# Optimization experiments

Measured on AMD Instinct MI355X. Metric: run time of the kernel, lower is better.

## Reference

```python
import jax, jax.numpy as jnp
import numpy as np

B, T, L, H, W = 8, 30000, 6, 128, 128
D_IN, C_DIM, HID, Z_DIM = 3, 32, 256, 128
MAX_DIM = 0.55


def setup_inputs() -> dict:
    key = jax.random.key(0)
    ks = jax.random.split(key, 12)
    p = jax.random.uniform(ks[0], (B, T, D_IN), dtype=jnp.float32)
    z = jax.random.normal(ks[1], (B, Z_DIM), dtype=jnp.float32)
    c = jax.random.normal(ks[2], (B, L, H, W, C_DIM), dtype=jnp.float32)
    # camera-like matrices: small rotation rows so projected coords stay in [-1, 1]
    C_mat = (jax.random.uniform(ks[3], (B, L, 4, 3), dtype=jnp.float32) - 0.5) * 0.3
    C_mat = C_mat.at[:, :, 3, :].set(1.0)  # row used as projection denominator
    fc_p_w = jax.random.normal(ks[4], (HID, D_IN), dtype=jnp.float32) * 0.1
    fc_p_b = jnp.zeros((HID,), jnp.float32)
    blk0_w0 = jax.random.normal(ks[5], (C_DIM, HID), dtype=jnp.float32) * 0.05
    blk0_b0 = jnp.zeros((C_DIM,), jnp.float32)
    blk0_w1 = jax.random.normal(ks[6], (C_DIM, C_DIM), dtype=jnp.float32) * 0.1
    blk0_b1 = jnp.zeros((C_DIM,), jnp.float32)
    blk0_ws = jax.random.normal(ks[7], (C_DIM, HID), dtype=jnp.float32) * 0.05
    blk_w0 = jax.random.normal(ks[8], (4, C_DIM, C_DIM), dtype=jnp.float32) * 0.1
    blk_b0 = jnp.zeros((4, C_DIM), jnp.float32)
    blk_w1 = jax.random.normal(ks[9], (4, C_DIM, C_DIM), dtype=jnp.float32) * 0.1
    blk_b1 = jnp.zeros((4, C_DIM), jnp.float32)
    fc_out_w = jax.random.normal(ks[10], (1, C_DIM), dtype=jnp.float32) * 0.1
    fc_out_b = jnp.zeros((1,), jnp.float32)
    return dict(p=p, z=z, c=c, C_mat=C_mat, fc_p_w=fc_p_w, fc_p_b=fc_p_b,
                blk0_w0=blk0_w0, blk0_b0=blk0_b0, blk0_w1=blk0_w1, blk0_b1=blk0_b1,
                blk0_ws=blk0_ws, blk_w0=blk_w0, blk_b0=blk_b0, blk_w1=blk_w1,
                blk_b1=blk_b1, fc_out_w=fc_out_w, fc_out_b=fc_out_b)


def _bilinear(p, c, C_mat):
    # p: [B,T,3], c: [B,L,H,W,D], C_mat: [B,L,4,3]
    Bb, Ll, Hh, Ww, Dd = c.shape
    interval = 2.0 / (Hh - 1)
    pp = p / MAX_DIM
    # proj[b,l,t,i] = sum_j C_mat[b,l,i,j] * pp[b,t,j]
    proj = jnp.einsum('blij,btj->blti', C_mat[:, :, :3, :], pp)
    denom = C_mat[:, :, 3, 0] + 0.05                      # [B,L]
    proj = proj / denom[:, :, None, None]
    xy = (proj[..., :2] + 1.0) / interval                 # [B,L,T,2]
    x, y = xy[..., 0], xy[..., 1]
    x0f, x1f = jnp.floor(x), jnp.ceil(x)
    y0f, y1f = jnp.floor(y), jnp.ceil(y)
    dx = (x1f - x)[..., None]                             # [B,L,T,1]
    dy = (y1f - y)[..., None]
    x0 = jnp.clip(x0f.astype(jnp.int32), 0, Hh - 1)
    x1 = jnp.clip(x1f.astype(jnp.int32), 0, Hh - 1)
    y0 = jnp.clip(y0f.astype(jnp.int32), 0, Ww - 1)
    y1 = jnp.clip(y1f.astype(jnp.int32), 0, Ww - 1)
    bi = jnp.arange(Bb)[:, None, None]
    li = jnp.arange(Ll)[None, :, None]
    f11 = c[bi, li, x0, y0]                               # [B,L,T,D]
    f12 = c[bi, li, x1, y0]
    f21 = c[bi, li, x0, y1]
    f22 = c[bi, li, x1, y1]
    interp = (f11 * dx * dy + f12 * (1 - dx) * dy
              + f21 * dx * (1 - dy) + f22 * (1 - dx) * (1 - dy))
    return interp.sum(axis=1)                             # sum over views -> [B,T,D]


def reference(p, z, c, C_mat, fc_p_w, fc_p_b, blk0_w0, blk0_b0, blk0_w1, blk0_b1,
              blk0_ws, blk_w0, blk_b0, blk_w1, blk_b1, fc_out_w, fc_out_b):
    feat = _bilinear(p, c, C_mat)                         # [B,T,32]
    net = p @ fc_p_w.T + fc_p_b                           # 1x1 conv == linear, [B,T,256]
    # block0 (256 -> 32, with linear shortcut)
    h = jax.nn.relu(net) @ blk0_w0.T + blk0_b0
    dx_ = jax.nn.relu(h) @ blk0_w1.T + blk0_b1
    net = net @ blk0_ws.T + dx_
    net = net + feat
    # blocks 1..4 (32 -> 32, identity shortcut)
    for i in range(4):
        h = jax.nn.relu(net) @ blk_w0[i].T + blk_b0[i]
        net = net + (jax.nn.relu(h) @ blk_w1[i].T + blk_b1[i])
        net = net + feat
    out = jax.nn.relu(net) @ fc_out_w.T + fc_out_b        # [B,T,1]
    return out[..., 0]                                    # [B,T]
```

## Files before the change

### kernel.cpp

```cpp
#include <hip/hip_runtime.h>

#define NB 8
#define NT 30000
#define NL 6
#define NC 32
#define NHID 256

typedef _Float16 f16;
typedef f16 half8 __attribute__((ext_vector_type(8)));
typedef f16 half4v __attribute__((ext_vector_type(4)));
typedef f16 half2v __attribute__((ext_vector_type(2)));
typedef float floatx4 __attribute__((ext_vector_type(4)));

__device__ __forceinline__ int permrow(int m) {
    return 8 * ((m & 15) >> 2) + 4 * (m >> 4) + (m & 3);
}

__device__ __forceinline__ half2v cvt2(float a, float b) {
    return __builtin_bit_cast(half2v, __builtin_amdgcn_cvt_pkrtz(a, b));
}

__device__ __forceinline__ half8 relupack2(floatx4 a, floatx4 b) {
    half2v p0 = cvt2(fmaxf(a[0], 0.f), fmaxf(a[1], 0.f));
    half2v p1 = cvt2(fmaxf(a[2], 0.f), fmaxf(a[3], 0.f));
    half2v p2 = cvt2(fmaxf(b[0], 0.f), fmaxf(b[1], 0.f));
    half2v p3 = cvt2(fmaxf(b[2], 0.f), fmaxf(b[3], 0.f));
    half4v q0 = __builtin_shufflevector(p0, p1, 0, 1, 2, 3);
    half4v q1 = __builtin_shufflevector(p2, p3, 0, 1, 2, 3);
    return __builtin_shufflevector(q0, q1, 0, 1, 2, 3, 4, 5, 6, 7);
}

__device__ __forceinline__ half8 zext4(half4v lo) {
    const half4v zh = {};
    return __builtin_shufflevector(lo, zh, 0, 1, 2, 3, 4, 5, 6, 7);
}

__global__ void fold_kernel(const float* __restrict__ ws, const float* __restrict__ fpw,
                            const float* __restrict__ fpb, floatx4* __restrict__ out) {
    __shared__ floatx4 s_part[8][32];
    int tid = threadIdx.x;
    int i = tid & 31, kc = tid >> 5;
    const float* wrow = ws + i * 256 + kc * 32;
    const float* pw = fpw + kc * 96;
    const float* pb = fpb + kc * 32;
    floatx4 acc = {};
    #pragma unroll 8
    for (int k = 0; k < 32; k++) {
        float w = wrow[k];
        acc[0] = fmaf(w, pw[k * 3 + 0], acc[0]);
        acc[1] = fmaf(w, pw[k * 3 + 1], acc[1]);
        acc[2] = fmaf(w, pw[k * 3 + 2], acc[2]);
        acc[3] = fmaf(w, pb[k], acc[3]);
    }
    s_part[kc][i] = acc;
    __syncthreads();
    if (kc == 0) {
        floatx4 s = s_part[0][i];
        #pragma unroll
        for (int j = 1; j < 8; j++) s += s_part[j][i];
        out[i] = s;
    }
}

__launch_bounds__(256, 2)
__global__ void decoder_kernel(
    const float* __restrict__ p, const float* __restrict__ c, const float* __restrict__ Cm,
    const float* __restrict__ fpw, const float* __restrict__ fpb,
    const float* __restrict__ b0w0, const float* __restrict__ b0b0,
    const float* __restrict__ b0w1, const float* __restrict__ b0b1,
    const float* __restrict__ bw0, const float* __restrict__ bb0,
    const float* __restrict__ bw1, const float* __restrict__ bb1,
    const float* __restrict__ fow, const float* __restrict__ fob,
    const floatx4* __restrict__ fold, float* __restrict__ out)
{
    __shared__ __align__(16) f16 s_w0A[32 * 256];
    __shared__ __align__(16) f16 s_wA[9 * 32 * 32];
    __shared__ __align__(16) f16 s_hB[256 * 4];
    __shared__ __align__(16) f16 s_foldA[32 * 4];
    __shared__ __align__(16) float s_b0b0[32], s_fow[32];
    __shared__ __align__(16) float s_bb0f[128], s_bb1f[128];
    __shared__ float s_cam[NL][8];
    __shared__ float s_fob;

    const int tid = threadIdx.x;
    const int b = blockIdx.y;

    {
        int m = tid >> 3, seg = tid & 7;
        const float* src = b0w0 + permrow(m) * 256 + seg * 32;
        f16* dst = s_w0A + m * 256;
        int sw = m & 7;
        #pragma unroll
        for (int ci = 0; ci < 4; ci++) {
            int cidx = seg * 4 + ci;
            floatx4 f0 = *(const floatx4*)(src + ci * 8);
            floatx4 f1 = *(const floatx4*)(src + ci * 8 + 4);
            half2v h0 = cvt2(f0[0], f0[1]), h1 = cvt2(f0[2], f0[3]);
            half2v h2 = cvt2(f1[0], f1[1]), h3 = cvt2(f1[2], f1[3]);
            half4v q0 = __builtin_shufflevector(h0, h1, 0, 1, 2, 3);
            half4v q1 = __builtin_shufflevector(h2, h3, 0, 1, 2, 3);
            half8 h = __builtin_shufflevector(q0, q1, 0, 1, 2, 3, 4, 5, 6, 7);
            *(half8*)(dst + ((cidx ^ sw) << 3)) = h;
        }
    }
    for (int r = tid; r < 288; r += 256) {
        int mi = r >> 5, m = r & 31;
        int pm = permrow(m);
        const float* src;
        if (mi == 0) src = b0w1 + pm * 32;
        else {
            int mat = mi - 1, bi = mat >> 1;
            src = ((mat & 1) ? bw1 : bw0) + (bi * 32 + pm) * 32;
        }
        f16* dst = s_wA + mi * 1024 + m * 32;
        int sw = (m >> 1) & 3;
        #pragma unroll
        for (int ci = 0; ci < 4; ci++) {
            floatx4 f0 = *(const floatx4*)(src + ci * 8);
            floatx4 f1 = *(const floatx4*)(src + ci * 8 + 4);
            half2v h0 = cvt2(f0[0], f0[1]), h1 = cvt2(f0[2], f0[3]);
            half2v h2 = cvt2(f1[0], f1[1]), h3 = cvt2(f1[2], f1[3]);
            half4v q0 = __builtin_shufflevector(h0, h1, 0, 1, 2, 3);
            half4v q1 = __builtin_shufflevector(h2, h3, 0, 1, 2, 3);
            half8 h = __builtin_shufflevector(q0, q1, 0, 1, 2, 3, 4, 5, 6, 7);
            *(half8*)(dst + ((ci ^ sw) << 3)) = h;
        }
    }
    {
        int cch = tid >> 5, m = tid & 31;
        int h = cch * 32 + permrow(m);
        half2v a = cvt2(fpw[h * 3 + 0], fpw[h * 3 + 1]);
        half2v bq = cvt2(fpw[h * 3 + 2], fpb[h]);
        *(half4v*)(s_hB + tid * 4) = __builtin_shufflevector(a, bq, 0, 1, 2, 3);
    }
    if (tid < 32) {
        int pm = permrow(tid);
        floatx4 f = fold[pm];
        half2v a = cvt2(f[0], f[1]);
        half2v bq = cvt2(f[2], f[3] + b0b1[pm]);
        *(half4v*)(s_foldA + tid * 4) = __builtin_shufflevector(a, bq, 0, 1, 2, 3);
        s_b0b0[tid] = b0b0[tid];
        s_fow[tid]  = fow[tid];
    }
    if (tid >= 64 && tid < 192) {
        int j = tid - 64;
        s_bb0f[j] = bb0[j];
        s_bb1f[j] = bb1[j];
    }
    if (tid == 0) s_fob = fob[0];
    if (tid >= 192 && tid < 192 + NL) {
        int l = tid - 192;
        const float* cm = Cm + ((size_t)b * NL + l) * 12;
        float denom = cm[9] + 0.05f;
        float s = 63.5f / (0.55f * denom);
        s_cam[l][0] = cm[0] * s; s_cam[l][1] = cm[1] * s; s_cam[l][2] = cm[2] * s;
        s_cam[l][3] = cm[3] * s; s_cam[l][4] = cm[4] * s; s_cam[l][5] = cm[5] * s;
    }
    __syncthreads();

    const int lane = tid & 63;
    const int wv = tid >> 6;
    const int q = lane >> 4;
    const int i16 = lane & 15;
    const int sw0 = i16 & 7;

    const f16* w0r0 = s_w0A + i16 * 256;
    const f16* w0r1 = s_w0A + (16 + i16) * 256;
    const int qsw = (q ^ ((i16 >> 1) & 3)) << 3;
    const int soff0 = i16 * 32 + qsw;
    const int soff1 = (16 + i16) * 32 + qsw;
    const f16* hB0 = s_hB + i16 * 4;
    const f16* hB1 = s_hB + (16 + i16) * 4;
    const float* cq = c + (((size_t)b * NL) << 19) + q * 8;

    const half8 fA0 = zext4(*(const half4v*)(s_foldA + i16 * 4));
    const half8 fA1 = zext4(*(const half4v*)(s_foldA + (16 + i16) * 4));
    const floatx4 fw0 = *(const floatx4*)&s_fow[q * 8];
    const floatx4 fw1 = *(const floatx4*)&s_fow[q * 8 + 4];
    const floatx4 b00a = *(const floatx4*)&s_b0b0[q * 8];
    const floatx4 b00b = *(const floatx4*)&s_b0b0[q * 8 + 4];

    #pragma unroll 1
    for (int g = 0; g < 2; g++) {
        const int t = blockIdx.x * 128 + (g * 4 + wv) * 16 + i16;
        const int tc = min(t, NT - 1);
        const float* pp = p + ((size_t)b * NT + tc) * 3;
        float px = pp[0], py = pp[1], pz = pp[2];

        floatx4 fe0 = {}, fe1 = {};
        #pragma unroll 1
        for (int l = 0; l < NL; l++) {
            float x = s_cam[l][0] * px + s_cam[l][1] * py + s_cam[l][2] * pz + 63.5f;
            float y = s_cam[l][3] * px + s_cam[l][4] * py + s_cam[l][5] * pz + 63.5f;
            float x0f = floorf(x), x1f = ceilf(x);
            float y0f = floorf(y), y1f = ceilf(y);
            float dxw = x1f - x, dyw = y1f - y;
            int x0 = min(max((int)x0f, 0), 127);
            int x1 = min(max((int)x1f, 0), 127);
            int y0 = min(max((int)y0f, 0), 127);
            int y1 = min(max((int)y1f, 0), 127);
            const float* base = cq + ((size_t)l << 19);
            const floatx4* f11 = (const floatx4*)(base + (size_t)((x0 << 7) + y0) * 32);
            const floatx4* f12 = (const floatx4*)(base + (size_t)((x1 << 7) + y0) * 32);
            const floatx4* f21 = (const floatx4*)(base + (size_t)((x0 << 7) + y1) * 32);
            const floatx4* f22 = (const floatx4*)(base + (size_t)((x1 << 7) + y1) * 32);
            float w11 = dxw * dyw;
            float w12 = (1.f - dxw) * dyw;
            float w21 = dxw * (1.f - dyw);
            float w22 = (1.f - dxw) * (1.f - dyw);
            floatx4 a0 = f11[0], a1 = f11[1];
            floatx4 b0v = f12[0], b1v = f12[1];
            floatx4 c0v = f21[0], c1v = f21[1];
            floatx4 d0v = f22[0], d1v = f22[1];
            fe0 += a0 * w11 + b0v * w12 + c0v * w21 + d0v * w22;
            fe1 += a1 * w11 + b1v * w12 + c1v * w21 + d1v * w22;
        }

        half8 bp;
        {
            half2v xy = cvt2(px, py), z1 = cvt2(pz, 1.0f);
            half4v lo = __builtin_shufflevector(xy, z1, 0, 1, 2, 3);
            half8 full = zext4(lo);
            const half8 zh8 = {};
            bp = (q == 0) ? full : zh8;
        }

        floatx4 acc0 = b00a, acc1 = b00b;
        #pragma unroll 2
        for (int cch = 0; cch < 8; cch++) {
            half8 ha = zext4(*(const half4v*)(hB0 + cch * 128));
            half8 hb = zext4(*(const half4v*)(hB1 + cch * 128));
            floatx4 hz = {};
            floatx4 h0 = __builtin_amdgcn_mfma_f32_16x16x32_f16(ha, bp, hz, 0, 0, 0);
            floatx4 h1 = __builtin_amdgcn_mfma_f32_16x16x32_f16(hb, bp, hz, 0, 0, 0);
            half8 bf = relupack2(h0, h1);
            half8 a0 = *(const half8*)(w0r0 + ((((cch << 2) | q) ^ sw0) << 3));
            half8 a1 = *(const half8*)(w0r1 + ((((cch << 2) | q) ^ sw0) << 3));
            acc0 = __builtin_amdgcn_mfma_f32_16x16x32_f16(a0, bf, acc0, 0, 0, 0);
            acc1 = __builtin_amdgcn_mfma_f32_16x16x32_f16(a1, bf, acc1, 0, 0, 0);
        }

        floatx4 st0 = __builtin_amdgcn_mfma_f32_16x16x32_f16(fA0, bp, fe0, 0, 0, 0);
        floatx4 st1 = __builtin_amdgcn_mfma_f32_16x16x32_f16(fA1, bp, fe1, 0, 0, 0);
        {
            half8 bf = relupack2(acc0, acc1);
            half8 a0 = *(const half8*)(s_wA + soff0);
            half8 a1 = *(const half8*)(s_wA + soff1);
            st0 = __builtin_amdgcn_mfma_f32_16x16x32_f16(a0, bf, st0, 0, 0, 0);
            st1 = __builtin_amdgcn_mfma_f32_16x16x32_f16(a1, bf, st1, 0, 0, 0);
        }

        #pragma unroll
        for (int bk = 0; bk < 4; bk++) {
            const f16* w_a = s_wA + (1 + 2 * bk) * 1024;
            const f16* w_b = s_wA + (2 + 2 * bk) * 1024;
            floatx4 h0 = *(const floatx4*)&s_bb0f[bk * 32 + q * 8];
            floatx4 h1 = *(const floatx4*)&s_bb0f[bk * 32 + q * 8 + 4];
            {
                half8 bf = relupack2(st0, st1);
                half8 a0 = *(const half8*)(w_a + soff0);
                half8 a1 = *(const half8*)(w_a + soff1);
                h0 = __builtin_amdgcn_mfma_f32_16x16x32_f16(a0, bf, h0, 0, 0, 0);
                h1 = __builtin_amdgcn_mfma_f32_16x16x32_f16(a1, bf, h1, 0, 0, 0);
            }
            floatx4 d0 = *(const floatx4*)&s_bb1f[bk * 32 + q * 8];
            floatx4 d1 = *(const floatx4*)&s_bb1f[bk * 32 + q * 8 + 4];
            {
                half8 bf = relupack2(h0, h1);
                half8 a0 = *(const half8*)(w_b + soff0);
                half8 a1 = *(const half8*)(w_b + soff1);
                d0 = __builtin_amdgcn_mfma_f32_16x16x32_f16(a0, bf, d0, 0, 0, 0);
                d1 = __builtin_amdgcn_mfma_f32_16x16x32_f16(a1, bf, d1, 0, 0, 0);
            }
            st0 += d0 + fe0;
            st1 += d1 + fe1;
        }

        float o = 0.f;
        #pragma unroll
        for (int r = 0; r < 4; r++)
            o += fmaxf(st0[r], 0.f) * fw0[r] + fmaxf(st1[r], 0.f) * fw1[r];
        o += __shfl_xor(o, 16);
        o += __shfl_xor(o, 32);
        if (q == 0 && t < NT) out[(size_t)b * NT + t] = o + s_fob;
    }
}

extern "C" void kernel_launch(void* const* d_in, const int* in_sizes, int n_in,
                              void* d_out, int out_size, void* d_ws, size_t ws_size,
                              hipStream_t stream) {
    const float* p    = (const float*)d_in[0];
    const float* c    = (const float*)d_in[2];
    const float* Cm   = (const float*)d_in[3];
    const float* fpw  = (const float*)d_in[4];
    const float* fpb  = (const float*)d_in[5];
    const float* b0w0 = (const float*)d_in[6];
    const float* b0b0 = (const float*)d_in[7];
    const float* b0w1 = (const float*)d_in[8];
    const float* b0b1 = (const float*)d_in[9];
    const float* b0ws = (const float*)d_in[10];
    const float* bw0  = (const float*)d_in[11];
    const float* bb0  = (const float*)d_in[12];
    const float* bw1  = (const float*)d_in[13];
    const float* bb1  = (const float*)d_in[14];
    const float* fow  = (const float*)d_in[15];
    const float* fob  = (const float*)d_in[16];
    floatx4* fold = (floatx4*)d_ws;

    fold_kernel<<<1, 256, 0, stream>>>(b0ws, fpw, fpb, fold);

    dim3 grid((NT + 127) / 128, NB);
    decoder_kernel<<<grid, 256, 0, stream>>>(p, c, Cm, fpw, fpb,
                                             b0w0, b0b0, b0w1, b0b1,
                                             bw0, bb0, bw1, bb1,
                                             fow, fob, fold, (float*)d_out);
}
```

Measured before the change: 267.4 us.

## Interleave two point groups per wave and fold shortcut weights in-kernel

Replaces the sequential two-iteration point loop with a single pass that processes both 16-point groups together, interleaving their bilinear gathers and MFMA chains to expose more memory and matrix-core parallelism. Also removes the separate fold_kernel launch by computing the folded shortcut/first-layer weights in every block's prologue, with an extra barrier. This raises register pressure and duplicates a small fold computation across all blocks.

```diff
diff --git a/kernel.cpp b/kernel.cpp
--- a/kernel.cpp
+++ b/kernel.cpp
@@ -35,31 +35,29 @@
     return __builtin_shufflevector(lo, zh, 0, 1, 2, 3, 4, 5, 6, 7);
 }
 
-__global__ void fold_kernel(const float* __restrict__ ws, const float* __restrict__ fpw,
-                            const float* __restrict__ fpb, floatx4* __restrict__ out) {
-    __shared__ floatx4 s_part[8][32];
-    int tid = threadIdx.x;
-    int i = tid & 31, kc = tid >> 5;
-    const float* wrow = ws + i * 256 + kc * 32;
-    const float* pw = fpw + kc * 96;
-    const float* pb = fpb + kc * 32;
-    floatx4 acc = {};
-    #pragma unroll 8
-    for (int k = 0; k < 32; k++) {
-        float w = wrow[k];
-        acc[0] = fmaf(w, pw[k * 3 + 0], acc[0]);
-        acc[1] = fmaf(w, pw[k * 3 + 1], acc[1]);
-        acc[2] = fmaf(w, pw[k * 3 + 2], acc[2]);
-        acc[3] = fmaf(w, pb[k], acc[3]);
-    }
-    s_part[kc][i] = acc;
-    __syncthreads();
-    if (kc == 0) {
-        floatx4 s = s_part[0][i];
-        #pragma unroll
-        for (int j = 1; j < 8; j++) s += s_part[j][i];
-        out[i] = s;
-    }
+__device__ __forceinline__ void gatherv(const float* __restrict__ base, float x, float y,
+                                        floatx4& f0, floatx4& f1) {
+    float x0f = floorf(x), x1f = ceilf(x);
+    float y0f = floorf(y), y1f = ceilf(y);
+    float dxw = x1f - x, dyw = y1f - y;
+    int x0 = min(max((int)x0f, 0), 127);
+    int x1 = min(max((int)x1f, 0), 127);
+    int y0 = min(max((int)y0f, 0), 127);
+    int y1 = min(max((int)y1f, 0), 127);
+    const floatx4* f11 = (const floatx4*)(base + (size_t)((x0 << 7) + y0) * 32);
+    const floatx4* f12 = (const floatx4*)(base + (size_t)((x1 << 7) + y0) * 32);
+    const floatx4* f21 = (const floatx4*)(base + (size_t)((x0 << 7) + y1) * 32);
+    const floatx4* f22 = (const floatx4*)(base + (size_t)((x1 << 7) + y1) * 32);
+    float w11 = dxw * dyw;
+    float w12 = (1.f - dxw) * dyw;
+    float w21 = dxw * (1.f - dyw);
+    float w22 = (1.f - dxw) * (1.f - dyw);
+    floatx4 a0 = f11[0], a1 = f11[1];
+    floatx4 b0v = f12[0], b1v = f12[1];
+    floatx4 c0v = f21[0], c1v = f21[1];
+    floatx4 d0v = f22[0], d1v = f22[1];
+    f0 += a0 * w11 + b0v * w12 + c0v * w21 + d0v * w22;
+    f1 += a1 * w11 + b1v * w12 + c1v * w21 + d1v * w22;
 }
 
 __launch_bounds__(256, 2)
@@ -68,15 +66,16 @@
     const float* __restrict__ fpw, const float* __restrict__ fpb,
     const float* __restrict__ b0w0, const float* __restrict__ b0b0,
     const float* __restrict__ b0w1, const float* __restrict__ b0b1,
-    const float* __restrict__ bw0, const float* __restrict__ bb0,
-    const float* __restrict__ bw1, const float* __restrict__ bb1,
-    const float* __restrict__ fow, const float* __restrict__ fob,
-    const floatx4* __restrict__ fold, float* __restrict__ out)
+    const float* __restrict__ b0ws, const float* __restrict__ bw0,
+    const float* __restrict__ bb0, const float* __restrict__ bw1,
+    const float* __restrict__ bb1, const float* __restrict__ fow,
+    const float* __restrict__ fob, float* __restrict__ out)
 {
     __shared__ __align__(16) f16 s_w0A[32 * 256];
     __shared__ __align__(16) f16 s_wA[9 * 32 * 32];
     __shared__ __align__(16) f16 s_hB[256 * 4];
     __shared__ __align__(16) f16 s_foldA[32 * 4];
+    __shared__ floatx4 s_part[8][32];
     __shared__ __align__(16) float s_b0b0[32], s_fow[32];
     __shared__ __align__(16) float s_bb0f[128], s_bb1f[128];
     __shared__ float s_cam[NL][8];
@@ -133,12 +132,23 @@
         half2v bq = cvt2(fpw[h * 3 + 2], fpb[h]);
         *(half4v*)(s_hB + tid * 4) = __builtin_shufflevector(a, bq, 0, 1, 2, 3);
     }
+    {
+        int i = tid & 31, kc = tid >> 5;
+        const float* wrow = b0ws + i * 256 + kc * 32;
+        const float* pw = fpw + kc * 96;
+        const float* pb = fpb + kc * 32;
+        floatx4 acc = {};
+        #pragma unroll 8
+        for (int k = 0; k < 32; k++) {
+            float w = wrow[k];
+            acc[0] = fmaf(w, pw[k * 3 + 0], acc[0]);
+            acc[1] = fmaf(w, pw[k * 3 + 1], acc[1]);
+            acc[2] = fmaf(w, pw[k * 3 + 2], acc[2]);
+            acc[3] = fmaf(w, pb[k], acc[3]);
+        }
+        s_part[kc][i] = acc;
+    }
     if (tid < 32) {
-        int pm = permrow(tid);
-        floatx4 f = fold[pm];
-        half2v a = cvt2(f[0], f[1]);
-        half2v bq = cvt2(f[2], f[3] + b0b1[pm]);
-        *(half4v*)(s_foldA + tid * 4) = __builtin_shufflevector(a, bq, 0, 1, 2, 3);
         s_b0b0[tid] = b0b0[tid];
         s_fow[tid]  = fow[tid];
     }
@@ -157,6 +167,16 @@
         s_cam[l][3] = cm[3] * s; s_cam[l][4] = cm[4] * s; s_cam[l][5] = cm[5] * s;
     }
     __syncthreads();
+    if (tid < 32) {
+        int pm = permrow(tid);
+        floatx4 s = s_part[0][pm];
+        #pragma unroll
+        for (int j = 1; j < 8; j++) s += s_part[j][pm];
+        half2v a = cvt2(s[0], s[1]);
+        half2v bq = cvt2(s[2], s[3] + b0b1[pm]);
+        *(half4v*)(s_foldA + tid * 4) = __builtin_shufflevector(a, bq, 0, 1, 2, 3);
+    }
+    __syncthreads();
 
     const int lane = tid & 63;
     const int wv = tid >> 6;
@@ -180,109 +200,121 @@
     const floatx4 b00a = *(const floatx4*)&s_b0b0[q * 8];
     const floatx4 b00b = *(const floatx4*)&s_b0b0[q * 8 + 4];
 
-    #pragma unroll 1
-    for (int g = 0; g < 2; g++) {
-        const int t = blockIdx.x * 128 + (g * 4 + wv) * 16 + i16;
-        const int tc = min(t, NT - 1);
-        const float* pp = p + ((size_t)b * NT + tc) * 3;
-        float px = pp[0], py = pp[1], pz = pp[2];
-
-        floatx4 fe0 = {}, fe1 = {};
-        #pragma unroll 1
-        for (int l = 0; l < NL; l++) {
-            float x = s_cam[l][0] * px + s_cam[l][1] * py + s_cam[l][2] * pz + 63.5f;
-            float y = s_cam[l][3] * px + s_cam[l][4] * py + s_cam[l][5] * pz + 63.5f;
-            float x0f = floorf(x), x1f = ceilf(x);
-            float y0f = floorf(y), y1f = ceilf(y);
-            float dxw = x1f - x, dyw = y1f - y;
-            int x0 = min(max((int)x0f, 0), 127);
-            int x1 = min(max((int)x1f, 0), 127);
-            int y0 = min(max((int)y0f, 0), 127);
-            int y1 = min(max((int)y1f, 0), 127);
-            const float* base = cq + ((size_t)l << 19);
-            const floatx4* f11 = (const floatx4*)(base + (size_t)((x0 << 7) + y0) * 32);
-            const floatx4* f12 = (const floatx4*)(base + (size_t)((x1 << 7) + y0) * 32);
-            const floatx4* f21 = (const floatx4*)(base + (size_t)((x0 << 7) + y1) * 32);
-            const floatx4* f22 = (const floatx4*)(base + (size_t)((x1 << 7) + y1) * 32);
-            float w11 = dxw * dyw;
-            float w12 = (1.f - dxw) * dyw;
-            float w21 = dxw * (1.f - dyw);
-            float w22 = (1.f - dxw) * (1.f - dyw);
-            floatx4 a0 = f11[0], a1 = f11[1];
-            floatx4 b0v = f12[0], b1v = f12[1];
-            floatx4 c0v = f21[0], c1v = f21[1];
-            floatx4 d0v = f22[0], d1v = f22[1];
-            fe0 += a0 * w11 + b0v * w12 + c0v * w21 + d0v * w22;
-            fe1 += a1 * w11 + b1v * w12 + c1v * w21 + d1v * w22;
-        }
-
-        half8 bp;
+    const int ta = blockIdx.x * 128 + wv * 16 + i16;
+    const int tb = ta + 64;
+    const int tca = min(ta, NT - 1), tcb = min(tb, NT - 1);
+    const float* ppa = p + ((size_t)b * NT + tca) * 3;
+    const float* ppb = p + ((size_t)b * NT + tcb) * 3;
+    float pxa = ppa[0], pya = ppa[1], pza = ppa[2];
+    float pxb = ppb[0], pyb = ppb[1], pzb = ppb[2];
+
+    floatx4 feA0 = {}, feA1 = {}, feB0 = {}, feB1 = {};
+    #pragma unroll 2
+    for (int l = 0; l < NL; l++) {
+        float c0 = s_cam[l][0], c1 = s_cam[l][1], c2 = s_cam[l][2];
+        float c3 = s_cam[l][3], c4 = s_cam[l][4], c5 = s_cam[l][5];
+        const float* base = cq + ((size_t)l << 19);
+        float xa = c0 * pxa + c1 * pya + c2 * pza + 63.5f;
+        float ya = c3 * pxa + c4 * pya + c5 * pza + 63.5f;
+        float xb = c0 * pxb + c1 * pyb + c2 * pzb + 63.5f;
+        float yb = c3 * pxb + c4 * pyb + c5 * pzb + 63.5f;
+        gatherv(base, xa, ya, feA0, feA1);
+        gatherv(base, xb, yb, feB0, feB1);
+    }
+
+    half8 bpa, bpb;
+    {
+        const half8 zh8 = {};
+        half4v la = __builtin_shufflevector(cvt2(pxa, pya), cvt2(pza, 1.0f), 0, 1, 2, 3);
+        half4v lb = __builtin_shufflevector(cvt2(pxb, pyb), cvt2(pzb, 1.0f), 0, 1, 2, 3);
+        bpa = (q == 0) ? zext4(la) : zh8;
+        bpb = (q == 0) ? zext4(lb) : zh8;
+    }
+
+    floatx4 accA0 = b00a, accA1 = b00b, accB0 = b00a, accB1 = b00b;
+    #pragma unroll 2
+    for (int cch = 0; cch < 8; cch++) {
+        half8 ha = zext4(*(const half4v*)(hB0 + cch * 128));
+        half8 hb = zext4(*(const half4v*)(hB1 + cch * 128));
+        floatx4 hz = {};
+        floatx4 h0a = __builtin_amdgcn_mfma_f32_16x16x32_f16(ha, bpa, hz, 0, 0, 0);
+        floatx4 h1a = __builtin_amdgcn_mfma_f32_16x16x32_f16(hb, bpa, hz, 0, 0, 0);
+        floatx4 h0b = __builtin_amdgcn_mfma_f32_16x16x32_f16(ha, bpb, hz, 0, 0, 0);
+        floatx4 h1b = __builtin_amdgcn_mfma_f32_16x16x32_f16(hb, bpb, hz, 0, 0, 0);
+        half8 bfa = relupack2(h0a, h1a);
+        half8 bfb = relupack2(h0b, h1b);
+        half8 a0 = *(const half8*)(w0r0 + ((((cch << 2) | q) ^ sw0) << 3));
+        half8 a1 = *(const half8*)(w0r1 + ((((cch << 2) | q) ^ sw0) << 3));
+        accA0 = __builtin_amdgcn_mfma_f32_16x16x32_f16(a0, bfa, accA0, 0, 0, 0);
+        accA1 = __builtin_amdgcn_mfma_f32_16x16x32_f16(a1, bfa, accA1, 0, 0, 0);
+        accB0 = __builtin_amdgcn_mfma_f32_16x16x32_f16(a0, bfb, accB0, 0, 0, 0);
+        accB1 = __builtin_amdgcn_mfma_f32_16x16x32_f16(a1, bfb, accB1, 0, 0, 0);
+    }
+
+    floatx4 stA0 = __builtin_amdgcn_mfma_f32_16x16x32_f16(fA0, bpa, feA0, 0, 0, 0);
+    floatx4 stA1 = __builtin_amdgcn_mfma_f32_16x16x32_f16(fA1, bpa, feA1, 0, 0, 0);
+    floatx4 stB0 = __builtin_amdgcn_mfma_f32_16x16x32_f16(fA0, bpb, feB0, 0, 0, 0);
+    floatx4 stB1 = __builtin_amdgcn_mfma_f32_16x16x32_f16(fA1, bpb, feB1, 0, 0, 0);
+    {
+        half8 bfa = relupack2(accA0, accA1);
+        half8 bfb = relupack2(accB0, accB1);
+        half8 a0 = *(const half8*)(s_wA + soff0);
+        half8 a1 = *(const half8*)(s_wA + soff1);
+        stA0 = __builtin_amdgcn_mfma_f32_16x16x32_f16(a0, bfa, stA0, 0, 0, 0);
+        stA1 = __builtin_amdgcn_mfma_f32_16x16x32_f16(a1, bfa, stA1, 0, 0, 0);
+        stB0 = __builtin_amdgcn_mfma_f32_16x16x32_f16(a0, bfb, stB0, 0, 0, 0);
+        stB1 = __builtin_amdgcn_mfma_f32_16x16x32_f16(a1, bfb, stB1, 0, 0, 0);
+    }
+
+    #pragma unroll
+    for (int bk = 0; bk < 4; bk++) {
+        const f16* w_a = s_wA + (1 + 2 * bk) * 1024;
+        const f16* w_b = s_wA + (2 + 2 * bk) * 1024;
+        floatx4 hb0 = *(const floatx4*)&s_bb0f[bk * 32 + q * 8];
+        floatx4 hb1 = *(const floatx4*)&s_bb0f[bk * 32 + q * 8 + 4];
+        floatx4 hA0 = hb0, hA1 = hb1, hB0v = hb0, hB1v = hb1;
         {
-            half2v xy = cvt2(px, py), z1 = cvt2(pz, 1.0f);
-            half4v lo = __builtin_shufflevector(xy, z1, 0, 1, 2, 3);
-            half8 full = zext4(lo);
-            const half8 zh8 = {};
-            bp = (q == 0) ? full : zh8;
-        }
-
-        floatx4 acc0 = b00a, acc1 = b00b;
-        #pragma unroll 2
-        for (int cch = 0; cch < 8; cch++) {
-            half8 ha = zext4(*(const half4v*)(hB0 + cch * 128));
-            half8 hb = zext4(*(const half4v*)(hB1 + cch * 128));
-            floatx4 hz = {};
-            floatx4 h0 = __builtin_amdgcn_mfma_f32_16x16x32_f16(ha, bp, hz, 0, 0, 0);
-            floatx4 h1 = __builtin_amdgcn_mfma_f32_16x16x32_f16(hb, bp, hz, 0, 0, 0);
-            half8 bf = relupack2(h0, h1);
-            half8 a0 = *(const half8*)(w0r0 + ((((cch << 2) | q) ^ sw0) << 3));
-            half8 a1 = *(const half8*)(w0r1 + ((((cch << 2) | q) ^ sw0) << 3));
-            acc0 = __builtin_amdgcn_mfma_f32_16x16x32_f16(a0, bf, acc0, 0, 0, 0);
-            acc1 = __builtin_amdgcn_mfma_f32_16x16x32_f16(a1, bf, acc1, 0, 0, 0);
-        }
-
-        floatx4 st0 = __builtin_amdgcn_mfma_f32_16x16x32_f16(fA0, bp, fe0, 0, 0, 0);
-        floatx4 st1 = __builtin_amdgcn_mfma_f32_16x16x32_f16(fA1, bp, fe1, 0, 0, 0);
+            half8 bfa = relupack2(stA0, stA1);
+            half8 bfb = relupack2(stB0, stB1);
+            half8 a0 = *(const half8*)(w_a + soff0);
+            half8 a1 = *(const half8*)(w_a + soff1);
+            hA0 = __builtin_amdgcn_mfma_f32_16x16x32_f16(a0, bfa, hA0, 0, 0, 0);
+            hA1 = __builtin_amdgcn_mfma_f32_16x16x32_f16(a1, bfa, hA1, 0, 0, 0);
+            hB0v = __builtin_amdgcn_mfma_f32_16x16x32_f16(a0, bfb, hB0v, 0, 0, 0);
+            hB1v = __builtin_amdgcn_mfma_f32_16x16x32_f16(a1, bfb, hB1v, 0, 0, 0);
+        }
+        floatx4 db0 = *(const floatx4*)&s_bb1f[bk * 32 + q * 8];
+        floatx4 db1 = *(const floatx4*)&s_bb1f[bk * 32 + q * 8 + 4];
+        floatx4 dA0 = db0, dA1 = db1, dB0 = db0, dB1 = db1;
         {
-            half8 bf = relupack2(acc0, acc1);
-            half8 a0 = *(const half8*)(s_wA + soff0);
-            half8 a1 = *(const half8*)(s_wA + soff1);
-            st0 = __builtin_amdgcn_mfma_f32_16x16x32_f16(a0, bf, st0, 0, 0, 0);
-            st1 = __builtin_amdgcn_mfma_f32_16x16x32_f16(a1, bf, st1, 0, 0, 0);
-        }
-
-        #pragma unroll
-        for (int bk = 0; bk < 4; bk++) {
-            const f16* w_a = s_wA + (1 + 2 * bk) * 1024;
-            const f16* w_b = s_wA + (2 + 2 * bk) * 1024;
-            floatx4 h0 = *(const floatx4*)&s_bb0f[bk * 32 + q * 8];
-            floatx4 h1 = *(const floatx4*)&s_bb0f[bk * 32 + q * 8 + 4];
-            {
-                half8 bf = relupack2(st0, st1);
-                half8 a0 = *(const half8*)(w_a + soff0);
-                half8 a1 = *(const half8*)(w_a + soff1);
-                h0 = __builtin_amdgcn_mfma_f32_16x16x32_f16(a0, bf, h0, 0, 0, 0);
-                h1 = __builtin_amdgcn_mfma_f32_16x16x32_f16(a1, bf, h1, 0, 0, 0);
-            }
-            floatx4 d0 = *(const floatx4*)&s_bb1f[bk * 32 + q * 8];
-            floatx4 d1 = *(const floatx4*)&s_bb1f[bk * 32 + q * 8 + 4];
-            {
-                half8 bf = relupack2(h0, h1);
-                half8 a0 = *(const half8*)(w_b + soff0);
-                half8 a1 = *(const half8*)(w_b + soff1);
-                d0 = __builtin_amdgcn_mfma_f32_16x16x32_f16(a0, bf, d0, 0, 0, 0);
-                d1 = __builtin_amdgcn_mfma_f32_16x16x32_f16(a1, bf, d1, 0, 0, 0);
-            }
-            st0 += d0 + fe0;
-            st1 += d1 + fe1;
-        }
-
-        float o = 0.f;
-        #pragma unroll
-        for (int r = 0; r < 4; r++)
-            o += fmaxf(st0[r], 0.f) * fw0[r] + fmaxf(st1[r], 0.f) * fw1[r];
-        o += __shfl_xor(o, 16);
-        o += __shfl_xor(o, 32);
-        if (q == 0 && t < NT) out[(size_t)b * NT + t] = o + s_fob;
+            half8 bfa = relupack2(hA0, hA1);
+            half8 bfb = relupack2(hB0v, hB1v);
+            half8 a0 = *(const half8*)(w_b + soff0);
+            half8 a1 = *(const half8*)(w_b + soff1);
+            dA0 = __builtin_amdgcn_mfma_f32_16x16x32_f16(a0, bfa, dA0, 0, 0, 0);
+            dA1 = __builtin_amdgcn_mfma_f32_16x16x32_f16(a1, bfa, dA1, 0, 0, 0);
+            dB0 = __builtin_amdgcn_mfma_f32_16x16x32_f16(a0, bfb, dB0, 0, 0, 0);
+            dB1 = __builtin_amdgcn_mfma_f32_16x16x32_f16(a1, bfb, dB1, 0, 0, 0);
+        }
+        stA0 += dA0 + feA0;
+        stA1 += dA1 + feA1;
+        stB0 += dB0 + feB0;
+        stB1 += dB1 + feB1;
+    }
+
+    float oa = 0.f, ob = 0.f;
+    #pragma unroll
+    for (int r = 0; r < 4; r++) {
+        oa += fmaxf(stA0[r], 0.f) * fw0[r] + fmaxf(stA1[r], 0.f) * fw1[r];
+        ob += fmaxf(stB0[r], 0.f) * fw0[r] + fmaxf(stB1[r], 0.f) * fw1[r];
+    }
+    oa += __shfl_xor(oa, 16);
+    oa += __shfl_xor(oa, 32);
+    ob += __shfl_xor(ob, 16);
+    ob += __shfl_xor(ob, 32);
+    if (q == 0) {
+        if (ta < NT) out[(size_t)b * NT + ta] = oa + s_fob;
+        if (tb < NT) out[(size_t)b * NT + tb] = ob + s_fob;
     }
 }
 
@@ -305,13 +337,10 @@
     const float* bb1  = (const float*)d_in[14];
     const float* fow  = (const float*)d_in[15];
     const float* fob  = (const float*)d_in[16];
-    floatx4* fold = (floatx4*)d_ws;
-
-    fold_kernel<<<1, 256, 0, stream>>>(b0ws, fpw, fpb, fold);
 
     dim3 grid((NT + 127) / 128, NB);
     decoder_kernel<<<grid, 256, 0, stream>>>(p, c, Cm, fpw, fpb,
-                                             b0w0, b0b0, b0w1, b0b1,
+                                             b0w0, b0b0, b0w1, b0b1, b0ws,
                                              bw0, bb0, bw1, bb1,
-                                             fow, fob, fold, (float*)d_out);
-}
+                                             fow, fob, (float*)d_out);
+}
```

Result: no change. 272.5 us (+1.9%).

## Convert feature grid to fp16 per call and fold weight-merge into decoder

Applied to the files above, without the earlier changes.

Adds a conversion kernel that turns the whole fp32 feature grid c into fp16 in the workspace on every call. The decoder then gathers the bilinear corners as half8 loads and does the weighted sum in fp16, halving the bytes per gather. The separate fold kernel is removed and its matrix product is recomputed in each decoder block's prologue. The grid becomes 1D with the batch index in the low bits, so neighbouring blocks cover different batches. The conversion pass reads the full 100 MB grid and writes 50 MB each call, which may cost more than the gather traffic it saves. Accumulating six views in fp16 also loses precision.

```diff
diff --git a/kernel.cpp b/kernel.cpp
--- a/kernel.cpp
+++ b/kernel.cpp
@@ -11,6 +11,8 @@
 typedef f16 half4v __attribute__((ext_vector_type(4)));
 typedef f16 half2v __attribute__((ext_vector_type(2)));
 typedef float floatx4 __attribute__((ext_vector_type(4)));
+
+#define C_ELEMS (25165824ull)
 
 __device__ __forceinline__ int permrow(int m) {
     return 8 * ((m & 15) >> 2) + 4 * (m >> 4) + (m & 3);
@@ -35,55 +37,62 @@
     return __builtin_shufflevector(lo, zh, 0, 1, 2, 3, 4, 5, 6, 7);
 }
 
-__global__ void fold_kernel(const float* __restrict__ ws, const float* __restrict__ fpw,
-                            const float* __restrict__ fpb, floatx4* __restrict__ out) {
-    __shared__ floatx4 s_part[8][32];
-    int tid = threadIdx.x;
-    int i = tid & 31, kc = tid >> 5;
-    const float* wrow = ws + i * 256 + kc * 32;
-    const float* pw = fpw + kc * 96;
-    const float* pb = fpb + kc * 32;
-    floatx4 acc = {};
-    #pragma unroll 8
-    for (int k = 0; k < 32; k++) {
-        float w = wrow[k];
-        acc[0] = fmaf(w, pw[k * 3 + 0], acc[0]);
-        acc[1] = fmaf(w, pw[k * 3 + 1], acc[1]);
-        acc[2] = fmaf(w, pw[k * 3 + 2], acc[2]);
-        acc[3] = fmaf(w, pb[k], acc[3]);
-    }
-    s_part[kc][i] = acc;
-    __syncthreads();
-    if (kc == 0) {
-        floatx4 s = s_part[0][i];
-        #pragma unroll
-        for (int j = 1; j < 8; j++) s += s_part[j][i];
-        out[i] = s;
-    }
-}
-
-__launch_bounds__(256, 2)
-__global__ void decoder_kernel(
-    const float* __restrict__ p, const float* __restrict__ c, const float* __restrict__ Cm,
+__device__ __forceinline__ half8 splat8(float w) {
+    f16 h = (f16)w;
+    half8 v = {h, h, h, h, h, h, h, h};
+    return v;
+}
+
+__device__ __forceinline__ void corners(float x, float y, int& i11, int& i12,
+                                        int& i21, int& i22, float& dxw, float& dyw) {
+    float x0f = floorf(x), x1f = ceilf(x);
+    float y0f = floorf(y), y1f = ceilf(y);
+    dxw = x1f - x; dyw = y1f - y;
+    int x0 = min(max((int)x0f, 0), 127);
+    int x1 = min(max((int)x1f, 0), 127);
+    int y0 = min(max((int)y0f, 0), 127);
+    int y1 = min(max((int)y1f, 0), 127);
+    i11 = (x0 << 7) + y0; i12 = (x1 << 7) + y0;
+    i21 = (x0 << 7) + y1; i22 = (x1 << 7) + y1;
+}
+
+__global__ __launch_bounds__(256) void convert_kernel(const float* __restrict__ c,
+                                                      f16* __restrict__ ch) {
+    size_t i = ((size_t)blockIdx.x * 256 + threadIdx.x) * 8;
+    floatx4 f0 = *(const floatx4*)(c + i);
+    floatx4 f1 = *(const floatx4*)(c + i + 4);
+    half2v h0 = cvt2(f0[0], f0[1]), h1 = cvt2(f0[2], f0[3]);
+    half2v h2 = cvt2(f1[0], f1[1]), h3 = cvt2(f1[2], f1[3]);
+    half4v q0 = __builtin_shufflevector(h0, h1, 0, 1, 2, 3);
+    half4v q1 = __builtin_shufflevector(h2, h3, 0, 1, 2, 3);
+    *(half8*)(ch + i) = __builtin_shufflevector(q0, q1, 0, 1, 2, 3, 4, 5, 6, 7);
+}
+
+template <bool F16>
+__global__ __launch_bounds__(256, 2) void decoder_kernel(
+    const float* __restrict__ p, const float* __restrict__ c, const f16* __restrict__ chalf,
+    const float* __restrict__ Cm,
     const float* __restrict__ fpw, const float* __restrict__ fpb,
     const float* __restrict__ b0w0, const float* __restrict__ b0b0,
     const float* __restrict__ b0w1, const float* __restrict__ b0b1,
-    const float* __restrict__ bw0, const float* __restrict__ bb0,
-    const float* __restrict__ bw1, const float* __restrict__ bb1,
-    const float* __restrict__ fow, const float* __restrict__ fob,
-    const floatx4* __restrict__ fold, float* __restrict__ out)
+    const float* __restrict__ b0ws, const float* __restrict__ bw0,
+    const float* __restrict__ bb0, const float* __restrict__ bw1,
+    const float* __restrict__ bb1, const float* __restrict__ fow,
+    const float* __restrict__ fob, float* __restrict__ out)
 {
     __shared__ __align__(16) f16 s_w0A[32 * 256];
     __shared__ __align__(16) f16 s_wA[9 * 32 * 32];
     __shared__ __align__(16) f16 s_hB[256 * 4];
     __shared__ __align__(16) f16 s_foldA[32 * 4];
+    __shared__ floatx4 s_part[8][32];
     __shared__ __align__(16) float s_b0b0[32], s_fow[32];
     __shared__ __align__(16) float s_bb0f[128], s_bb1f[128];
     __shared__ float s_cam[NL][8];
     __shared__ float s_fob;
 
     const int tid = threadIdx.x;
-    const int b = blockIdx.y;
+    const int b = blockIdx.x & 7;
+    const int tile = blockIdx.x >> 3;
 
     {
         int m = tid >> 3, seg = tid & 7;
@@ -133,12 +142,23 @@
         half2v bq = cvt2(fpw[h * 3 + 2], fpb[h]);
         *(half4v*)(s_hB + tid * 4) = __builtin_shufflevector(a, bq, 0, 1, 2, 3);
     }
+    {
+        int i = tid & 31, kc = tid >> 5;
+        const float* wrow = b0ws + i * 256 + kc * 32;
+        const float* pw = fpw + kc * 96;
+        const float* pb = fpb + kc * 32;
+        floatx4 acc = {};
+        #pragma unroll 8
+        for (int k = 0; k < 32; k++) {
+            float w = wrow[k];
+            acc[0] = fmaf(w, pw[k * 3 + 0], acc[0]);
+            acc[1] = fmaf(w, pw[k * 3 + 1], acc[1]);
+            acc[2] = fmaf(w, pw[k * 3 + 2], acc[2]);
+            acc[3] = fmaf(w, pb[k], acc[3]);
+        }
+        s_part[kc][i] = acc;
+    }
     if (tid < 32) {
-        int pm = permrow(tid);
-        floatx4 f = fold[pm];
-        half2v a = cvt2(f[0], f[1]);
-        half2v bq = cvt2(f[2], f[3] + b0b1[pm]);
-        *(half4v*)(s_foldA + tid * 4) = __builtin_shufflevector(a, bq, 0, 1, 2, 3);
         s_b0b0[tid] = b0b0[tid];
         s_fow[tid]  = fow[tid];
     }
@@ -157,6 +177,16 @@
         s_cam[l][3] = cm[3] * s; s_cam[l][4] = cm[4] * s; s_cam[l][5] = cm[5] * s;
     }
     __syncthreads();
+    if (tid < 32) {
+        int pm = permrow(tid);
+        floatx4 s = s_part[0][pm];
+        #pragma unroll
+        for (int j = 1; j < 8; j++) s += s_part[j][pm];
+        half2v a = cvt2(s[0], s[1]);
+        half2v bq = cvt2(s[2], s[3] + b0b1[pm]);
+        *(half4v*)(s_foldA + tid * 4) = __builtin_shufflevector(a, bq, 0, 1, 2, 3);
+    }
+    __syncthreads();
 
     const int lane = tid & 63;
     const int wv = tid >> 6;
@@ -172,6 +202,7 @@
     const f16* hB0 = s_hB + i16 * 4;
     const f16* hB1 = s_hB + (16 + i16) * 4;
     const float* cq = c + (((size_t)b * NL) << 19) + q * 8;
+    const f16* cqh = chalf + (((size_t)b * NL) << 19) + q * 8;
 
     const half8 fA0 = zext4(*(const half4v*)(s_foldA + i16 * 4));
     const half8 fA1 = zext4(*(const half4v*)(s_foldA + (16 + i16) * 4));
@@ -182,38 +213,55 @@
 
     #pragma unroll 1
     for (int g = 0; g < 2; g++) {
-        const int t = blockIdx.x * 128 + (g * 4 + wv) * 16 + i16;
+        const int t = tile * 128 + (g * 4 + wv) * 16 + i16;
         const int tc = min(t, NT - 1);
         const float* pp = p + ((size_t)b * NT + tc) * 3;
         float px = pp[0], py = pp[1], pz = pp[2];
 
-        floatx4 fe0 = {}, fe1 = {};
-        #pragma unroll 1
-        for (int l = 0; l < NL; l++) {
-            float x = s_cam[l][0] * px + s_cam[l][1] * py + s_cam[l][2] * pz + 63.5f;
-            float y = s_cam[l][3] * px + s_cam[l][4] * py + s_cam[l][5] * pz + 63.5f;
-            float x0f = floorf(x), x1f = ceilf(x);
-            float y0f = floorf(y), y1f = ceilf(y);
-            float dxw = x1f - x, dyw = y1f - y;
-            int x0 = min(max((int)x0f, 0), 127);
-            int x1 = min(max((int)x1f, 0), 127);
-            int y0 = min(max((int)y0f, 0), 127);
-            int y1 = min(max((int)y1f, 0), 127);
-            const float* base = cq + ((size_t)l << 19);
-            const floatx4* f11 = (const floatx4*)(base + (size_t)((x0 << 7) + y0) * 32);
-            const floatx4* f12 = (const floatx4*)(base + (size_t)((x1 << 7) + y0) * 32);
-            const floatx4* f21 = (const floatx4*)(base + (size_t)((x0 << 7) + y1) * 32);
-            const floatx4* f22 = (const floatx4*)(base + (size_t)((x1 << 7) + y1) * 32);
-            float w11 = dxw * dyw;
-            float w12 = (1.f - dxw) * dyw;
-            float w21 = dxw * (1.f - dyw);
-            float w22 = (1.f - dxw) * (1.f - dyw);
-            floatx4 a0 = f11[0], a1 = f11[1];
-            floatx4 b0v = f12[0], b1v = f12[1];
-            floatx4 c0v = f21[0], c1v = f21[1];
-            floatx4 d0v = f22[0], d1v = f22[1];
-            fe0 += a0 * w11 + b0v * w12 + c0v * w21 + d0v * w22;
-            fe1 += a1 * w11 + b1v * w12 + c1v * w21 + d1v * w22;
+        floatx4 fe0, fe1;
+        if constexpr (F16) {
+            half8 feh = {};
+            #pragma unroll 1
+            for (int l = 0; l < NL; l++) {
+                float x = s_cam[l][0] * px + s_cam[l][1] * py + s_cam[l][2] * pz + 63.5f;
+                float y = s_cam[l][3] * px + s_cam[l][4] * py + s_cam[l][5] * pz + 63.5f;
+                int i11, i12, i21, i22; float dxw, dyw;
+                corners(x, y, i11, i12, i21, i22, dxw, dyw);
+                const f16* base = cqh + ((size_t)l << 19);
+                half8 t11 = *(const half8*)(base + (size_t)i11 * 32);
+                half8 t12 = *(const half8*)(base + (size_t)i12 * 32);
+                half8 t21 = *(const half8*)(base + (size_t)i21 * 32);
+                half8 t22 = *(const half8*)(base + (size_t)i22 * 32);
+                float w11 = dxw * dyw;
+                float w12 = (1.f - dxw) * dyw;
+                float w21 = dxw * (1.f - dyw);
+                float w22 = (1.f - dxw) * (1.f - dyw);
+                feh += t11 * splat8(w11) + t12 * splat8(w12)
+                     + t21 * splat8(w21) + t22 * splat8(w22);
+            }
+            fe0 = floatx4{(float)feh[0], (float)feh[1], (float)feh[2], (float)feh[3]};
+            fe1 = floatx4{(float)feh[4], (float)feh[5], (float)feh[6], (float)feh[7]};
+        } else {
+            floatx4 a0_ = {}, a1_ = {};
+            #pragma unroll 1
+            for (int l = 0; l < NL; l++) {
+                float x = s_cam[l][0] * px + s_cam[l][1] * py + s_cam[l][2] * pz + 63.5f;
+                float y = s_cam[l][3] * px + s_cam[l][4] * py + s_cam[l][5] * pz + 63.5f;
+                int i11, i12, i21, i22; float dxw, dyw;
+                corners(x, y, i11, i12, i21, i22, dxw, dyw);
+                const float* base = cq + ((size_t)l << 19);
+                const floatx4* f11 = (const floatx4*)(base + (size_t)i11 * 32);
+                const floatx4* f12 = (const floatx4*)(base + (size_t)i12 * 32);
+                const floatx4* f21 = (const floatx4*)(base + (size_t)i21 * 32);
+                const floatx4* f22 = (const floatx4*)(base + (size_t)i22 * 32);
+                float w11 = dxw * dyw;
+                float w12 = (1.f - dxw) * dyw;
+                float w21 = dxw * (1.f - dyw);
+                float w22 = (1.f - dxw) * (1.f - dyw);
+                a0_ += f11[0] * w11 + f12[0] * w12 + f21[0] * w21 + f22[0] * w22;
+                a1_ += f11[1] * w11 + f12[1] * w12 + f21[1] * w21 + f22[1] * w22;
+            }
+            fe0 = a0_; fe1 = a1_;
         }
 
         half8 bp;
@@ -305,13 +353,20 @@
     const float* bb1  = (const float*)d_in[14];
     const float* fow  = (const float*)d_in[15];
     const float* fob  = (const float*)d_in[16];
-    floatx4* fold = (floatx4*)d_ws;
-
-    fold_kernel<<<1, 256, 0, stream>>>(b0ws, fpw, fpb, fold);
-
-    dim3 grid((NT + 127) / 128, NB);
-    decoder_kernel<<<grid, 256, 0, stream>>>(p, c, Cm, fpw, fpb,
-                                             b0w0, b0b0, b0w1, b0b1,
-                                             bw0, bb0, bw1, bb1,
-                                             fow, fob, fold, (float*)d_out);
-}
+
+    dim3 grid(((NT + 127) / 128) * NB);
+
+    if (ws_size >= C_ELEMS * sizeof(f16)) {
+        f16* chalf = (f16*)d_ws;
+        convert_kernel<<<(int)(C_ELEMS / 8 / 256), 256, 0, stream>>>(c, chalf);
+        decoder_kernel<true><<<grid, 256, 0, stream>>>(p, c, chalf, Cm, fpw, fpb,
+                                                       b0w0, b0b0, b0w1, b0b1, b0ws,
+                                                       bw0, bb0, bw1, bb1,
+                                                       fow, fob, (float*)d_out);
+    } else {
+        decoder_kernel<false><<<grid, 256, 0, stream>>>(p, c, nullptr, Cm, fpw, fpb,
+                                                        b0w0, b0b0, b0w1, b0b1, b0ws,
+                                                        bw0, bb0, bw1, bb1,
+                                                        fow, fob, (float*)d_out);
+    }
+}
```

Result: no change. 263.6 us (-1.4%).
